# Performance work log

Measured on AMD Instinct MI355X. Metric: run time of the kernel, lower is better.

Reference implementation:

```python
import jax, jax.numpy as jnp
import numpy as np

NTOKEN = 150000   # len(ui2idx)
NINP   = 64       # opt.d_word_vec
NHID   = 2 * NINP # gnn1 output dim
NEDGE  = 2400000  # hetero static graph edges
B, L   = 64, 200  # batch_size, max_len


def setup_inputs() -> dict:
    key = jax.random.key(0)
    ks = jax.random.split(key, 8)
    def xavier(k, shape):
        scale = (2.0 / (shape[0] + shape[1])) ** 0.5
        return scale * jax.random.normal(k, shape, jnp.float32)
    emb = xavier(ks[0], (NTOKEN, NINP)).at[0].set(0.0)  # padding_idx=0
    W1 = xavier(ks[1], (NINP, NHID))
    b1 = jnp.zeros((NHID,), jnp.float32)
    W2 = xavier(ks[2], (NHID, NINP))
    b2 = jnp.zeros((NINP,), jnp.float32)
    edge_index = jax.random.randint(ks[3], (2, NEDGE), 0, NTOKEN, dtype=jnp.int32).astype(jnp.int64)
    inp = jax.random.randint(ks[4], (B, L), 0, NTOKEN, dtype=jnp.int32).astype(jnp.int64)
    input_timestamp = jax.random.randint(ks[5], (B, L), 0, 300000, dtype=jnp.int32).astype(jnp.int64)
    return {"emb": emb, "W1": W1, "b1": b1, "W2": W2, "b2": b2,
            "input": inp, "input_timestamp": input_timestamp, "edge_index": edge_index}


def gcn_conv(x, W, b, src, dst, n):
    # torch_geometric GCNConv: out = D^{-1/2}(A+I)D^{-1/2} (x W) + b
    h = x @ W                                   # [n, out]
    deg = jnp.zeros((n,), h.dtype).at[dst].add(1.0) + 1.0  # +1 self-loop
    dinv = jax.lax.rsqrt(deg)
    norm = dinv[src] * dinv[dst]                # [E]
    agg = jax.ops.segment_sum(h[src] * norm[:, None], dst, num_segments=n)
    return agg + h * (dinv * dinv)[:, None] + b  # self-loop term + bias


def reference(emb, W1, b1, W2, b2, input, input_timestamp, edge_index):
    src, dst = edge_index[0], edge_index[1]
    h = gcn_conv(emb, W1, b1, src, dst, NTOKEN)      # dropout is identity in eval
    nodes = gcn_conv(h, W2, b2, src, dst, NTOKEN)    # [NTOKEN, NINP]
    # one-hot scatter + einsum 'bt,td->bd' == direct gather
    b_, l_ = input.shape
    return nodes[input.reshape(-1)].reshape(b_, l_, NINP)
```

## Files before the change

kernel.cpp:

```cpp
#include <hip/hip_runtime.h>
#include <hip/hip_bf16.h>

#define NTOKEN 150000
#define NINP   64
#define NEDGE  2400000
#define NPOS   (64*200)

#define NPB    256
#define NBUCK  586
#define EPB    8192
#define NBLK   293
#define CAP    4608

#define NXB    1172

#define O_XBF      0
#define O_Z1       4800000
#define O_HIST     4800000
#define O_BUCK     9600000
#define O_CTOT     12000000
#define O_BST      12000640
#define O_DINV     12001280
#define O_RS       12151296
#define O_M        12451328
#define O_CVEC     12455424

__device__ __forceinline__ unsigned f2bf(float f) {
    unsigned u = __float_as_uint(f);
    return (u + 0x7FFFu + ((u >> 16) & 1u)) >> 16;
}

__global__ void __launch_bounds__(1024) k1(
        const float4* __restrict__ X4, uint4* __restrict__ Xbf,
        const int4* __restrict__ dst4, int* __restrict__ histG,
        const float* __restrict__ W1, const float* __restrict__ b1,
        const float* __restrict__ W2, float* __restrict__ M,
        float* __restrict__ cvec) {
    __shared__ int h[NBUCK];
    int t = threadIdx.x, B = blockIdx.x;
    if (B < NXB) {
        int i = B * 1024 + t;
        if (i < NTOKEN * 64 / 8) {
            float4 a = X4[2 * i], b = X4[2 * i + 1];
            uint4 o;
            o.x = f2bf(a.x) | (f2bf(a.y) << 16);
            o.y = f2bf(a.z) | (f2bf(a.w) << 16);
            o.z = f2bf(b.x) | (f2bf(b.y) << 16);
            o.w = f2bf(b.z) | (f2bf(b.w) << 16);
            Xbf[i] = o;
        }
    } else if (B < NXB + NBLK) {
        int hb = B - NXB;
        for (int i = t; i < NBUCK; i += 1024) h[i] = 0;
        __syncthreads();
        int base4 = hb * (EPB / 4);
        #pragma unroll
        for (int it = 0; it < EPB / 4096; it++) {
            int idx = base4 + it * 1024 + t;
            if (idx < NEDGE / 4) {
                int4 d = dst4[idx];
                atomicAdd(&h[d.x >> 8], 1);
                atomicAdd(&h[d.y >> 8], 1);
                atomicAdd(&h[d.z >> 8], 1);
                atomicAdd(&h[d.w >> 8], 1);
            }
        }
        __syncthreads();
        for (int i = t; i < NBUCK; i += 1024) histG[hb * NBUCK + i] = h[i];
    } else if (B < NXB + NBLK + 4) {
        int o = (B - NXB - NBLK) * 1024 + t;
        int i = o >> 6, j = o & 63;
        float s = 0.f;
        #pragma unroll 4
        for (int k = 0; k < 128; k++) s = fmaf(W1[i * 128 + k], W2[k * 64 + j], s);
        M[o] = s;
    } else if (t < 64) {
        float s = 0.f;
        #pragma unroll 4
        for (int k = 0; k < 128; k++) s = fmaf(b1[k], W2[k * 64 + t], s);
        cvec[t] = s;
    }
}

__global__ void kB1_colscan(int* __restrict__ histG, int* __restrict__ colTotal) {
    __shared__ int sd[256];
    int t = threadIdx.x, b = blockIdx.x;
    int i0 = 2 * t, i1 = 2 * t + 1;
    int v0 = (i0 < NBLK) ? histG[i0 * NBUCK + b] : 0;
    int v1 = (i1 < NBLK) ? histG[i1 * NBUCK + b] : 0;
    int tsum = v0 + v1;
    sd[t] = tsum;
    __syncthreads();
    for (int off = 1; off < 256; off <<= 1) {
        int x = (t >= off) ? sd[t - off] : 0;
        __syncthreads();
        sd[t] += x;
        __syncthreads();
    }
    int excl = sd[t] - tsum;
    if (i0 < NBLK) histG[i0 * NBUCK + b] = excl;
    if (i1 < NBLK) histG[i1 * NBUCK + b] = excl + v0;
    if (t == 255) colTotal[b] = sd[255];
}

__global__ void __launch_bounds__(1024) kC_scatter(
        const int4* __restrict__ src4, const int4* __restrict__ dst4,
        const int* __restrict__ histG, const int* __restrict__ colTotal,
        int* __restrict__ bsG, int* __restrict__ bucketPacked) {
    __shared__ int sd[1024];
    __shared__ int bs[NBUCK + 1];
    __shared__ int cur[NBUCK];
    int t = threadIdx.x, B = blockIdx.x;
    int v0 = (t < NBUCK) ? colTotal[t] : 0;
    sd[t] = v0;
    __syncthreads();
    for (int off = 1; off < 1024; off <<= 1) {
        int x = (t >= off) ? sd[t - off] : 0;
        __syncthreads();
        sd[t] += x;
        __syncthreads();
    }
    if (t < NBUCK) bs[t] = sd[t] - v0;
    if (t == 0) bs[NBUCK] = NEDGE;
    __syncthreads();
    if (B == 0)
        for (int i = t; i < NBUCK + 1; i += 1024) bsG[i] = bs[i];
    for (int i = t; i < NBUCK; i += 1024) cur[i] = histG[B * NBUCK + i] + bs[i];
    __syncthreads();
    int base4 = B * (EPB / 4);
    #pragma unroll
    for (int it = 0; it < EPB / 4096; it++) {
        int idx = base4 + it * 1024 + t;
        if (idx < NEDGE / 4) {
            int4 s = src4[idx];
            int4 d = dst4[idx];
            int p0 = atomicAdd(&cur[d.x >> 8], 1);
            bucketPacked[p0] = (s.x << 8) | (d.x & 255);
            int p1 = atomicAdd(&cur[d.y >> 8], 1);
            bucketPacked[p1] = (s.y << 8) | (d.y & 255);
            int p2 = atomicAdd(&cur[d.z >> 8], 1);
            bucketPacked[p2] = (s.z << 8) | (d.z & 255);
            int p3 = atomicAdd(&cur[d.w >> 8], 1);
            bucketPacked[p3] = (s.w << 8) | (d.w & 255);
        }
    }
}

__global__ void __launch_bounds__(1024) kDS(
        const int* __restrict__ bsG,
        int* __restrict__ bucketPacked ,
        float* __restrict__ dinv, int* __restrict__ rowStart) {
    __shared__ int srt[CAP];
    __shared__ int cnt[NPB];
    __shared__ int sd[NPB];
    int t = threadIdx.x, b = blockIdx.x;
    int e0 = bsG[b], e1 = bsG[b + 1], nE = e1 - e0;
    int nEc = (nE < CAP) ? nE : CAP;
    if (t < NPB) cnt[t] = 0;
    __syncthreads();
    for (int i = t; i < nEc; i += 1024) atomicAdd(&cnt[bucketPacked[e0 + i] & 255], 1);
    __syncthreads();
    int c = 0;
    if (t < NPB) { c = cnt[t]; sd[t] = c; }
    __syncthreads();
    for (int off = 1; off < 256; off <<= 1) {
        int x = 0;
        if (t < NPB && t >= off) x = sd[t - off];
        __syncthreads();
        if (t < NPB) sd[t] += x;
        __syncthreads();
    }
    if (t < NPB) {
        int excl = sd[t] - c;
        cnt[t] = excl;
        int node = b * NPB + t;
        if (node < NTOKEN) {
            dinv[node] = rsqrtf((float)c + 1.0f);
            rowStart[node] = e0 + excl;
        }
        if (b == NBUCK - 1 && t == 0) rowStart[NTOKEN] = NEDGE;
    }
    __syncthreads();
    for (int i = t; i < nEc; i += 1024) {
        int p = bucketPacked[e0 + i];
        int pos = atomicAdd(&cnt[p & 255], 1);
        if (pos < CAP) srt[pos] = p >> 8;
    }
    __syncthreads();
    for (int i = t; i < nEc; i += 1024) bucketPacked[e0 + i] = srt[i];
}

__global__ void k_agg(const uint2* __restrict__ Xb, const float* __restrict__ dinv,
                      const int* __restrict__ rowStart, const int* __restrict__ sortedSrc,
                      uint2* __restrict__ Z1b) {
    int g = threadIdx.x >> 4;
    int fl = threadIdx.x & 15;
    int v = blockIdx.x * 16 + g;
    int e0 = rowStart[v], e1 = rowStart[v + 1];
    float dv = dinv[v];
    uint2 xsw = Xb[(size_t)v * 16 + fl];
    float a0x=0.f,a0y=0.f,a0z=0.f,a0w=0.f, a1x=0.f,a1y=0.f,a1z=0.f,a1w=0.f;
    float a2x=0.f,a2y=0.f,a2z=0.f,a2w=0.f, a3x=0.f,a3y=0.f,a3z=0.f,a3w=0.f;
    for (int e = e0; e < e1; e += 8) {
        int m1=e+1<e1, m2=e+2<e1, m3=e+3<e1, m4=e+4<e1, m5=e+5<e1, m6=e+6<e1, m7=e+7<e1;
        int u0 = sortedSrc[e];
        int u1 = sortedSrc[m1 ? e+1 : e];
        int u2 = sortedSrc[m2 ? e+2 : e];
        int u3 = sortedSrc[m3 ? e+3 : e];
        int u4 = sortedSrc[m4 ? e+4 : e];
        int u5 = sortedSrc[m5 ? e+5 : e];
        int u6 = sortedSrc[m6 ? e+6 : e];
        int u7 = sortedSrc[m7 ? e+7 : e];
        float d0 = dinv[u0];
        float d1 = m1 ? dinv[u1] : 0.f;
        float d2 = m2 ? dinv[u2] : 0.f;
        float d3 = m3 ? dinv[u3] : 0.f;
        float d4 = m4 ? dinv[u4] : 0.f;
        float d5 = m5 ? dinv[u5] : 0.f;
        float d6 = m6 ? dinv[u6] : 0.f;
        float d7 = m7 ? dinv[u7] : 0.f;
        uint2 w0 = Xb[(size_t)u0 * 16 + fl];
        uint2 w1 = Xb[(size_t)u1 * 16 + fl];
        uint2 w2 = Xb[(size_t)u2 * 16 + fl];
        uint2 w3 = Xb[(size_t)u3 * 16 + fl];
        uint2 w4 = Xb[(size_t)u4 * 16 + fl];
        uint2 w5 = Xb[(size_t)u5 * 16 + fl];
        uint2 w6 = Xb[(size_t)u6 * 16 + fl];
        uint2 w7 = Xb[(size_t)u7 * 16 + fl];
        #define ACC(d,w,AX,AY,AZ,AW) \
            AX = fmaf(d, __uint_as_float((w).x << 16), AX); \
            AY = fmaf(d, __uint_as_float((w).x & 0xFFFF0000u), AY); \
            AZ = fmaf(d, __uint_as_float((w).y << 16), AZ); \
            AW = fmaf(d, __uint_as_float((w).y & 0xFFFF0000u), AW);
        ACC(d0,w0,a0x,a0y,a0z,a0w)
        ACC(d1,w1,a1x,a1y,a1z,a1w)
        ACC(d2,w2,a2x,a2y,a2z,a2w)
        ACC(d3,w3,a3x,a3y,a3z,a3w)
        ACC(d4,w4,a0x,a0y,a0z,a0w)
        ACC(d5,w5,a1x,a1y,a1z,a1w)
        ACC(d6,w6,a2x,a2y,a2z,a2w)
        ACC(d7,w7,a3x,a3y,a3z,a3w)
        #undef ACC
    }
    float ax = (a0x + a1x) + (a2x + a3x);
    float ay = (a0y + a1y) + (a2y + a3y);
    float az = (a0z + a1z) + (a2z + a3z);
    float aw = (a0w + a1w) + (a2w + a3w);
    float c = dv * dv;
    float ox = c * fmaf(dv, __uint_as_float(xsw.x << 16),         ax);
    float oy = c * fmaf(dv, __uint_as_float(xsw.x & 0xFFFF0000u), ay);
    float oz = c * fmaf(dv, __uint_as_float(xsw.y << 16),         az);
    float ow = c * fmaf(dv, __uint_as_float(xsw.y & 0xFFFF0000u), aw);
    uint2 o;
    o.x = f2bf(ox) | (f2bf(oy) << 16);
    o.y = f2bf(oz) | (f2bf(ow) << 16);
    Z1b[(size_t)v * 16 + fl] = o;
}

__global__ void k_out(const int* __restrict__ inp, const uint2* __restrict__ Z1b,
                      const float* __restrict__ dinv, const int* __restrict__ rowStart,
                      const int* __restrict__ sortedSrc, const float* __restrict__ M,
                      const float* __restrict__ cvec, const float* __restrict__ b2,
                      float* __restrict__ out) {
    int wid = threadIdx.x >> 6;
    int lane = threadIdx.x & 63;
    int g = lane >> 4, fl = lane & 15;
    int p = blockIdx.x * 4 + wid;
    if (p >= NPOS) return;
    int v = inp[p];
    int e0 = rowStart[v], e1 = rowStart[v + 1];
    float ax0=0.f,ay0=0.f,az0=0.f,aw0=0.f,ss0=0.f;
    float ax1=0.f,ay1=0.f,az1=0.f,aw1=0.f,ss1=0.f;
    int e = e0 + g;
    for (; e + 4 < e1; e += 8) {
        int u0 = sortedSrc[e];
        int u1 = sortedSrc[e + 4];
        ss0 += dinv[u0]; ss1 += dinv[u1];
        uint2 z0 = Z1b[(size_t)u0 * 16 + fl];
        uint2 z1 = Z1b[(size_t)u1 * 16 + fl];
        ax0 += __uint_as_float(z0.x << 16);
        ay0 += __uint_as_float(z0.x & 0xFFFF0000u);
        az0 += __uint_as_float(z0.y << 16);
        aw0 += __uint_as_float(z0.y & 0xFFFF0000u);
        ax1 += __uint_as_float(z1.x << 16);
        ay1 += __uint_as_float(z1.x & 0xFFFF0000u);
        az1 += __uint_as_float(z1.y << 16);
        aw1 += __uint_as_float(z1.y & 0xFFFF0000u);
    }
    if (e < e1) {
        int u = sortedSrc[e];
        ss0 += dinv[u];
        uint2 z = Z1b[(size_t)u * 16 + fl];
        ax0 += __uint_as_float(z.x << 16);
        ay0 += __uint_as_float(z.x & 0xFFFF0000u);
        az0 += __uint_as_float(z.y << 16);
        aw0 += __uint_as_float(z.y & 0xFFFF0000u);
    }
    float ax = ax0 + ax1, ay = ay0 + ay1, az = az0 + az1, aw = aw0 + aw1, ss = ss0 + ss1;
    ax += __shfl_xor(ax, 16, 64); ay += __shfl_xor(ay, 16, 64);
    az += __shfl_xor(az, 16, 64); aw += __shfl_xor(aw, 16, 64);
    ss += __shfl_xor(ss, 16, 64);
    ax += __shfl_xor(ax, 32, 64); ay += __shfl_xor(ay, 32, 64);
    az += __shfl_xor(az, 32, 64); aw += __shfl_xor(aw, 32, 64);
    ss += __shfl_xor(ss, 32, 64);
    float dv = dinv[v];
    uint2 zs = Z1b[(size_t)v * 16 + fl];
    float z2x = dv * (ax + __uint_as_float(zs.x << 16));
    float z2y = dv * (ay + __uint_as_float(zs.x & 0xFFFF0000u));
    float z2z = dv * (az + __uint_as_float(zs.y << 16));
    float z2w = dv * (aw + __uint_as_float(zs.y & 0xFFFF0000u));
    float s = dv * (ss + dv);
    float o = fmaf(s, cvec[lane], b2[lane]);
    #pragma unroll
    for (int kb = 0; kb < 16; kb++) {
        float a0 = __shfl(z2x, kb, 64);
        float a1 = __shfl(z2y, kb, 64);
        float a2 = __shfl(z2z, kb, 64);
        float a3 = __shfl(z2w, kb, 64);
        o = fmaf(a0, M[(kb * 4 + 0) * 64 + lane], o);
        o = fmaf(a1, M[(kb * 4 + 1) * 64 + lane], o);
        o = fmaf(a2, M[(kb * 4 + 2) * 64 + lane], o);
        o = fmaf(a3, M[(kb * 4 + 3) * 64 + lane], o);
    }
    out[(size_t)p * 64 + lane] = o;
}

extern "C" void kernel_launch(void* const* d_in, const int* in_sizes, int n_in,
                              void* d_out, int out_size, void* d_ws, size_t ws_size,
                              hipStream_t stream) {
    const float* emb = (const float*)d_in[0];
    const float* W1  = (const float*)d_in[1];
    const float* b1  = (const float*)d_in[2];
    const float* W2  = (const float*)d_in[3];
    const float* b2  = (const float*)d_in[4];
    const int*   inp = (const int*)d_in[5];
    const int*   ei  = (const int*)d_in[7];
    const int* srcArr = ei;
    const int* dstArr = ei + NEDGE;
    float* out = (float*)d_out;

    float* ws         = (float*)d_ws;
    uint2* Xbf        = (uint2*)(ws + O_XBF);
    uint2* Z1b        = (uint2*)(ws + O_Z1);
    int*   histG      = (int*)ws + O_HIST;
    int*   buckPacked = (int*)ws + O_BUCK;
    int*   colTotal   = (int*)ws + O_CTOT;
    int*   bsG        = (int*)ws + O_BST;
    float* dinv       = ws + O_DINV;
    int*   rowStart   = (int*)ws + O_RS;
    float* M          = ws + O_M;
    float* cvec       = ws + O_CVEC;

    k1         <<<NXB + NBLK + 5, 1024, 0, stream>>>((const float4*)emb, (uint4*)Xbf,
                                                     (const int4*)dstArr, histG,
                                                     W1, b1, W2, M, cvec);
    kB1_colscan<<<NBUCK, 256,  0, stream>>>(histG, colTotal);
    kC_scatter <<<NBLK,  1024, 0, stream>>>((const int4*)srcArr, (const int4*)dstArr,
                                            histG, colTotal, bsG, buckPacked);
    kDS        <<<NBUCK, 1024, 0, stream>>>(bsG, buckPacked, dinv, rowStart);
    k_agg      <<<NTOKEN/16, 256, 0, stream>>>(Xbf, dinv, rowStart, buckPacked, Z1b);
    k_out      <<<NPOS/4, 256, 0, stream>>>(inp, Z1b, dinv, rowStart,
                                            buckPacked, M, cvec, b2, out);
}
```

Before: 132.6 us.

## Replace two-pass histogram/scan bucketing with fixed-capacity buckets and global atomic reservation

Drops the separate dst histogram pass, the column-scan kernel and the prefix scan in the scatter. Each block now stages its edges in shared memory, builds a local bucket histogram, and reserves space with one global atomicAdd per bucket into fixed-stride buckets of CAP slots. The aim is to cut two launches and one extra read of the destination array. In exchange, the bucketed array holds padding slots filled with a dummy node (NTOKEN, which gets zeroed features and dinv = 0), so the aggregation kernels read that padding too. Edges are silently lost if a bucket ever exceeds CAP.

```diff
diff --git a/kernel.cpp b/kernel.cpp
--- a/kernel.cpp
+++ b/kernel.cpp
@@ -8,22 +8,20 @@
 
 #define NPB    256
 #define NBUCK  586
-#define EPB    8192
-#define NBLK   293
+#define EPB    4096
+#define NBLK   586
 #define CAP    4608
 
 #define NXB    1172
 
 #define O_XBF      0
-#define O_Z1       4800000
-#define O_HIST     4800000
-#define O_BUCK     9600000
-#define O_CTOT     12000000
-#define O_BST      12000640
-#define O_DINV     12001280
-#define O_RS       12151296
-#define O_M        12451328
-#define O_CVEC     12455424
+#define O_Z1       4800064
+#define O_BUCK     9600128
+#define O_GCUR     12300416
+#define O_DINV     12301056
+#define O_RS       12451072
+#define O_M        12601088
+#define O_CVEC     12605184
 
 __device__ __forceinline__ unsigned f2bf(float f) {
     unsigned u = __float_as_uint(f);
@@ -32,11 +30,10 @@
 
 __global__ void __launch_bounds__(1024) k1(
         const float4* __restrict__ X4, uint4* __restrict__ Xbf,
-        const int4* __restrict__ dst4, int* __restrict__ histG,
         const float* __restrict__ W1, const float* __restrict__ b1,
         const float* __restrict__ W2, float* __restrict__ M,
-        float* __restrict__ cvec) {
-    __shared__ int h[NBUCK];
+        float* __restrict__ cvec, int* __restrict__ gcur,
+        uint2* __restrict__ Z1b) {
     int t = threadIdx.x, B = blockIdx.x;
     if (B < NXB) {
         int i = B * 1024 + t;
@@ -49,116 +46,81 @@
             o.w = f2bf(b.z) | (f2bf(b.w) << 16);
             Xbf[i] = o;
         }
-    } else if (B < NXB + NBLK) {
-        int hb = B - NXB;
-        for (int i = t; i < NBUCK; i += 1024) h[i] = 0;
-        __syncthreads();
-        int base4 = hb * (EPB / 4);
-        #pragma unroll
-        for (int it = 0; it < EPB / 4096; it++) {
-            int idx = base4 + it * 1024 + t;
-            if (idx < NEDGE / 4) {
-                int4 d = dst4[idx];
-                atomicAdd(&h[d.x >> 8], 1);
-                atomicAdd(&h[d.y >> 8], 1);
-                atomicAdd(&h[d.z >> 8], 1);
-                atomicAdd(&h[d.w >> 8], 1);
-            }
-        }
-        __syncthreads();
-        for (int i = t; i < NBUCK; i += 1024) histG[hb * NBUCK + i] = h[i];
-    } else if (B < NXB + NBLK + 4) {
-        int o = (B - NXB - NBLK) * 1024 + t;
+    } else if (B < NXB + 4) {
+        int o = (B - NXB) * 1024 + t;
         int i = o >> 6, j = o & 63;
         float s = 0.f;
         #pragma unroll 4
         for (int k = 0; k < 128; k++) s = fmaf(W1[i * 128 + k], W2[k * 64 + j], s);
         M[o] = s;
-    } else if (t < 64) {
-        float s = 0.f;
-        #pragma unroll 4
-        for (int k = 0; k < 128; k++) s = fmaf(b1[k], W2[k * 64 + t], s);
-        cvec[t] = s;
-    }
-}
-
-__global__ void kB1_colscan(int* __restrict__ histG, int* __restrict__ colTotal) {
-    __shared__ int sd[256];
-    int t = threadIdx.x, b = blockIdx.x;
-    int i0 = 2 * t, i1 = 2 * t + 1;
-    int v0 = (i0 < NBLK) ? histG[i0 * NBUCK + b] : 0;
-    int v1 = (i1 < NBLK) ? histG[i1 * NBUCK + b] : 0;
-    int tsum = v0 + v1;
-    sd[t] = tsum;
-    __syncthreads();
-    for (int off = 1; off < 256; off <<= 1) {
-        int x = (t >= off) ? sd[t - off] : 0;
-        __syncthreads();
-        sd[t] += x;
-        __syncthreads();
-    }
-    int excl = sd[t] - tsum;
-    if (i0 < NBLK) histG[i0 * NBUCK + b] = excl;
-    if (i1 < NBLK) histG[i1 * NBUCK + b] = excl + v0;
-    if (t == 255) colTotal[b] = sd[255];
-}
-
-__global__ void __launch_bounds__(1024) kC_scatter(
+    } else if (B == NXB + 4) {
+        if (t < 64) {
+            float s = 0.f;
+            #pragma unroll 4
+            for (int k = 0; k < 128; k++) s = fmaf(b1[k], W2[k * 64 + t], s);
+            cvec[t] = s;
+        }
+    } else {
+        if (t < NBUCK) gcur[t] = t * CAP;
+        else if (t >= 586 && t < 594) {
+            uint4 z = {0u, 0u, 0u, 0u};
+            Xbf[(size_t)NTOKEN * 8 + (t - 586)] = z;
+        } else if (t >= 594 && t < 610) {
+            uint2 z = {0u, 0u};
+            Z1b[(size_t)NTOKEN * 16 + (t - 594)] = z;
+        }
+    }
+}
+
+__global__ void __launch_bounds__(512) kC(
         const int4* __restrict__ src4, const int4* __restrict__ dst4,
-        const int* __restrict__ histG, const int* __restrict__ colTotal,
-        int* __restrict__ bsG, int* __restrict__ bucketPacked) {
-    __shared__ int sd[1024];
-    __shared__ int bs[NBUCK + 1];
-    __shared__ int cur[NBUCK];
+        int* __restrict__ gcur, int* __restrict__ bucketPacked) {
+    __shared__ int eS[EPB];
+    __shared__ int eD[EPB];
+    __shared__ int h[NBUCK];
     int t = threadIdx.x, B = blockIdx.x;
-    int v0 = (t < NBUCK) ? colTotal[t] : 0;
-    sd[t] = v0;
-    __syncthreads();
-    for (int off = 1; off < 1024; off <<= 1) {
-        int x = (t >= off) ? sd[t - off] : 0;
-        __syncthreads();
-        sd[t] += x;
-        __syncthreads();
-    }
-    if (t < NBUCK) bs[t] = sd[t] - v0;
-    if (t == 0) bs[NBUCK] = NEDGE;
-    __syncthreads();
-    if (B == 0)
-        for (int i = t; i < NBUCK + 1; i += 1024) bsG[i] = bs[i];
-    for (int i = t; i < NBUCK; i += 1024) cur[i] = histG[B * NBUCK + i] + bs[i];
+    for (int i = t; i < NBUCK; i += 512) h[i] = 0;
     __syncthreads();
     int base4 = B * (EPB / 4);
-    #pragma unroll
-    for (int it = 0; it < EPB / 4096; it++) {
-        int idx = base4 + it * 1024 + t;
-        if (idx < NEDGE / 4) {
-            int4 s = src4[idx];
-            int4 d = dst4[idx];
-            int p0 = atomicAdd(&cur[d.x >> 8], 1);
-            bucketPacked[p0] = (s.x << 8) | (d.x & 255);
-            int p1 = atomicAdd(&cur[d.y >> 8], 1);
-            bucketPacked[p1] = (s.y << 8) | (d.y & 255);
-            int p2 = atomicAdd(&cur[d.z >> 8], 1);
-            bucketPacked[p2] = (s.z << 8) | (d.z & 255);
-            int p3 = atomicAdd(&cur[d.w >> 8], 1);
-            bucketPacked[p3] = (s.w << 8) | (d.w & 255);
-        }
-    }
-}
-
-__global__ void __launch_bounds__(1024) kDS(
-        const int* __restrict__ bsG,
+    int n4 = NEDGE / 4 - base4; if (n4 > EPB / 4) n4 = EPB / 4;
+    for (int i = t; i < n4; i += 512) {
+        int4 s = src4[base4 + i];
+        int4 d = dst4[base4 + i];
+        eS[4*i+0] = s.x; eS[4*i+1] = s.y; eS[4*i+2] = s.z; eS[4*i+3] = s.w;
+        eD[4*i+0] = d.x; eD[4*i+1] = d.y; eD[4*i+2] = d.z; eD[4*i+3] = d.w;
+        atomicAdd(&h[d.x >> 8], 1);
+        atomicAdd(&h[d.y >> 8], 1);
+        atomicAdd(&h[d.z >> 8], 1);
+        atomicAdd(&h[d.w >> 8], 1);
+    }
+    __syncthreads();
+    for (int b = t; b < NBUCK; b += 512) {
+        int c = h[b];
+        if (c) h[b] = atomicAdd(&gcur[b], c);
+    }
+    __syncthreads();
+    int n = n4 * 4;
+    for (int i = t; i < n; i += 512) {
+        int d = eD[i];
+        int b = d >> 8;
+        int pos = atomicAdd(&h[b], 1);
+        bucketPacked[pos] = (eS[i] << 8) | (d & 255);
+    }
+}
+
+__global__ void __launch_bounds__(512) kDS(
+        const int* __restrict__ gcur,
         int* __restrict__ bucketPacked ,
         float* __restrict__ dinv, int* __restrict__ rowStart) {
     __shared__ int srt[CAP];
     __shared__ int cnt[NPB];
     __shared__ int sd[NPB];
     int t = threadIdx.x, b = blockIdx.x;
-    int e0 = bsG[b], e1 = bsG[b + 1], nE = e1 - e0;
-    int nEc = (nE < CAP) ? nE : CAP;
+    int e0 = b * CAP;
+    int nE = gcur[b] - e0;
     if (t < NPB) cnt[t] = 0;
     __syncthreads();
-    for (int i = t; i < nEc; i += 1024) atomicAdd(&cnt[bucketPacked[e0 + i] & 255], 1);
+    for (int i = t; i < nE; i += 512) atomicAdd(&cnt[bucketPacked[e0 + i] & 255], 1);
     __syncthreads();
     int c = 0;
     if (t < NPB) { c = cnt[t]; sd[t] = c; }
@@ -178,16 +140,20 @@
             dinv[node] = rsqrtf((float)c + 1.0f);
             rowStart[node] = e0 + excl;
         }
-        if (b == NBUCK - 1 && t == 0) rowStart[NTOKEN] = NEDGE;
-    }
-    __syncthreads();
-    for (int i = t; i < nEc; i += 1024) {
+    }
+    if (b == 0 && t == 0) {
+        rowStart[NTOKEN] = NBUCK * CAP;
+        dinv[NTOKEN] = 0.f;
+    }
+    __syncthreads();
+    for (int i = t; i < nE; i += 512) {
         int p = bucketPacked[e0 + i];
         int pos = atomicAdd(&cnt[p & 255], 1);
         if (pos < CAP) srt[pos] = p >> 8;
     }
     __syncthreads();
-    for (int i = t; i < nEc; i += 1024) bucketPacked[e0 + i] = srt[i];
+    for (int i = t; i < nE; i += 512) bucketPacked[e0 + i] = srt[i];
+    for (int i = nE + t; i < CAP; i += 512) bucketPacked[e0 + i] = NTOKEN;
 }
 
 __global__ void k_agg(const uint2* __restrict__ Xb, const float* __restrict__ dinv,
@@ -342,23 +308,19 @@
     float* ws         = (float*)d_ws;
     uint2* Xbf        = (uint2*)(ws + O_XBF);
     uint2* Z1b        = (uint2*)(ws + O_Z1);
-    int*   histG      = (int*)ws + O_HIST;
     int*   buckPacked = (int*)ws + O_BUCK;
-    int*   colTotal   = (int*)ws + O_CTOT;
-    int*   bsG        = (int*)ws + O_BST;
+    int*   gcur       = (int*)ws + O_GCUR;
     float* dinv       = ws + O_DINV;
     int*   rowStart   = (int*)ws + O_RS;
     float* M          = ws + O_M;
     float* cvec       = ws + O_CVEC;
 
-    k1         <<<NXB + NBLK + 5, 1024, 0, stream>>>((const float4*)emb, (uint4*)Xbf,
-                                                     (const int4*)dstArr, histG,
-                                                     W1, b1, W2, M, cvec);
-    kB1_colscan<<<NBUCK, 256,  0, stream>>>(histG, colTotal);
-    kC_scatter <<<NBLK,  1024, 0, stream>>>((const int4*)srcArr, (const int4*)dstArr,
-                                            histG, colTotal, bsG, buckPacked);
-    kDS        <<<NBUCK, 1024, 0, stream>>>(bsG, buckPacked, dinv, rowStart);
-    k_agg      <<<NTOKEN/16, 256, 0, stream>>>(Xbf, dinv, rowStart, buckPacked, Z1b);
-    k_out      <<<NPOS/4, 256, 0, stream>>>(inp, Z1b, dinv, rowStart,
-                                            buckPacked, M, cvec, b2, out);
-}
+    k1    <<<NXB + 6, 1024, 0, stream>>>((const float4*)emb, (uint4*)Xbf,
+                                         W1, b1, W2, M, cvec, gcur, Z1b);
+    kC    <<<NBLK, 512, 0, stream>>>((const int4*)srcArr, (const int4*)dstArr,
+                                     gcur, buckPacked);
+    kDS   <<<NBUCK, 512, 0, stream>>>(gcur, buckPacked, dinv, rowStart);
+    k_agg <<<NTOKEN/16, 256, 0, stream>>>(Xbf, dinv, rowStart, buckPacked, Z1b);
+    k_out <<<NPOS/4, 256, 0, stream>>>(inp, Z1b, dinv, rowStart,
+                                       buckPacked, M, cvec, b2, out);
+}
```

Result: slower. 380.6 us (+187.0%).
